# Optimization experiments

Hardware: AMD Instinct MI355X
Metric: run time of the kernel (lower is better)

Reference implementation:

```python
import jax, jax.numpy as jnp
import numpy as np

MARGIN = 1.0
EPS = 1e-8


def setup_inputs() -> dict:
    key = jax.random.key(0)
    k1, k2 = jax.random.split(key)
    B, D, NUM_CLASSES = 8192, 512, 100
    features = jax.random.normal(k1, (B, D), dtype=jnp.float32)
    labels = jax.random.randint(k2, (B,), 0, NUM_CLASSES, dtype=jnp.int64)
    return {"features": features, "labels": labels}


def _metric_tensor(features):
    # G = I + feature covariance (curvature-aware metric on the feature manifold)
    B, D = features.shape
    centered = features - jnp.mean(features, axis=0, keepdims=True)
    cov = jnp.einsum('bi,bj->ij', centered, centered) / jnp.float32(B)
    return jnp.eye(D, dtype=features.dtype) + cov


def _masked_random_idx(mask, key):
    # gumbel-max trick: uniform random index among True entries of each row of mask [B,B]
    g = -jnp.log(-jnp.log(jax.random.uniform(key, mask.shape, dtype=jnp.float32) + EPS) + EPS)
    scores = jnp.where(mask, g, -jnp.inf)
    return jnp.argmax(scores, axis=1)


def reference(features, labels):
    B = features.shape[0]
    G = _metric_tensor(features)

    same = labels[:, None] == labels[None, :]              # [B,B]
    not_self = ~jnp.eye(B, dtype=bool)
    pos_mask = same & not_self
    neg_mask = ~same

    kp, kn = jax.random.split(jax.random.key(42))
    pos_idx = _masked_random_idx(pos_mask, kp)             # [B]
    neg_idx = _masked_random_idx(neg_mask, kn)             # [B]
    valid = jnp.any(pos_mask, axis=1) & jnp.any(neg_mask, axis=1)

    diff_p = features - features[pos_idx]                  # [B,D]
    diff_n = features - features[neg_idx]                  # [B,D]
    # Riemannian distance: sqrt((x-y)^T G (x-y))
    d_pos = jnp.sqrt(jnp.einsum('bi,ij,bj->b', diff_p, G, diff_p) + EPS)
    d_neg = jnp.sqrt(jnp.einsum('bi,ij,bj->b', diff_n, G, diff_n) + EPS)

    per_sample = jnp.maximum(d_pos - d_neg + MARGIN, 0.0)
    per_sample = jnp.where(valid, per_sample, 0.0)
    n_valid = jnp.maximum(jnp.sum(valid.astype(jnp.float32)), 1.0)
    return jnp.sum(per_sample) / n_valid
```

## Files before the change

### kernel.cpp

```cpp
#include <hip/hip_runtime.h>
#include <stdint.h>

#define BSZ   8192
#define DIM   512

typedef __attribute__((ext_vector_type(8))) short short8;
typedef __attribute__((ext_vector_type(4))) float f32x4;
typedef __attribute__((ext_vector_type(8))) uint16_t u16x8;

__host__ __device__ inline uint16_t f2bf(float x) {
  uint32_t u = __float_as_uint(x);
  return (uint16_t)((u + 0x7FFFu + ((u >> 16) & 1u)) >> 16);
}
__host__ __device__ inline float bf2f(uint16_t h) {
  return __uint_as_float(((uint32_t)h) << 16);
}

__host__ __device__ inline uint32_t rotl32(uint32_t v, int s) {
#if defined(__HIP_DEVICE_COMPILE__) && __has_builtin(__builtin_amdgcn_alignbit)
  return __builtin_amdgcn_alignbit(v, v, 32 - s);
#else
  return (v << s) | (v >> (32 - s));
#endif
}

__host__ __device__ inline void threefry2x32(uint32_t k0, uint32_t k1,
                                             uint32_t x0, uint32_t x1,
                                             uint32_t& o0, uint32_t& o1) {
  uint32_t ks2 = k0 ^ k1 ^ 0x1BD11BDAu;
  x0 += k0; x1 += k1;
  x0 += x1; x1 = rotl32(x1, 13); x1 ^= x0;
  x0 += x1; x1 = rotl32(x1, 15); x1 ^= x0;
  x0 += x1; x1 = rotl32(x1, 26); x1 ^= x0;
  x0 += x1; x1 = rotl32(x1,  6); x1 ^= x0;
  x0 += k1; x1 += ks2 + 1u;
  x0 += x1; x1 = rotl32(x1, 17); x1 ^= x0;
  x0 += x1; x1 = rotl32(x1, 29); x1 ^= x0;
  x0 += x1; x1 = rotl32(x1, 16); x1 ^= x0;
  x0 += x1; x1 = rotl32(x1, 24); x1 ^= x0;
  x0 += ks2; x1 += k0 + 2u;
  x0 += x1; x1 = rotl32(x1, 13); x1 ^= x0;
  x0 += x1; x1 = rotl32(x1, 15); x1 ^= x0;
  x0 += x1; x1 = rotl32(x1, 26); x1 ^= x0;
  x0 += x1; x1 = rotl32(x1,  6); x1 ^= x0;
  x0 += k0; x1 += k1 + 3u;
  x0 += x1; x1 = rotl32(x1, 17); x1 ^= x0;
  x0 += x1; x1 = rotl32(x1, 29); x1 ^= x0;
  x0 += x1; x1 = rotl32(x1, 16); x1 ^= x0;
  x0 += x1; x1 = rotl32(x1, 24); x1 ^= x0;
  x0 += k1; x1 += ks2 + 4u;
  x0 += x1; x1 = rotl32(x1, 13); x1 ^= x0;
  x0 += x1; x1 = rotl32(x1, 15); x1 ^= x0;
  x0 += x1; x1 = rotl32(x1, 26); x1 ^= x0;
  x0 += x1; x1 = rotl32(x1,  6); x1 ^= x0;
  x0 += ks2; x1 += k0 + 5u;
  o0 = x0; o1 = x1;
}

constexpr size_t OFF_ACC    = 0;
constexpr size_t OFF_S      = 1024;
constexpr size_t OFF_BSTART = 3072;
constexpr size_t OFF_BIDX   = 4096;
constexpr size_t OFF_PIDX   = 36864;
constexpr size_t OFF_NIDX   = 69632;
constexpr size_t OFF_LPART  = 102400;
constexpr size_t OFF_GB     = 131072;
constexpr size_t OFF_FB     = 2097152;
constexpr size_t OFF_HB     = 10485760;
constexpr size_t ZERO_BYTES = 3072;

__global__ __launch_bounds__(256) void convert_kernel(const float* __restrict__ F,
                                                      uint16_t* __restrict__ Fb) {
  int i = (blockIdx.x * 256 + threadIdx.x) * 8;
  float4 a = *(const float4*)&F[i];
  float4 b = *(const float4*)&F[i + 4];
  u16x8 o;
  o[0] = f2bf(a.x); o[1] = f2bf(a.y); o[2] = f2bf(a.z); o[3] = f2bf(a.w);
  o[4] = f2bf(b.x); o[5] = f2bf(b.y); o[6] = f2bf(b.z); o[7] = f2bf(b.w);
  *(u16x8*)&Fb[i] = o;
}

__global__ __launch_bounds__(256) void colsum_kernel(const float* __restrict__ F,
                                                     float* __restrict__ S) {
  int b0 = blockIdx.x * 32;
  int t = threadIdx.x;
  float s0 = 0.f, s1 = 0.f;
  for (int r = 0; r < 32; ++r) {
    const float* row = F + (size_t)(b0 + r) * DIM;
    s0 += row[t];
    s1 += row[t + 256];
  }
  atomicAdd(&S[t], s0);
  atomicAdd(&S[t + 256], s1);
}

__global__ __launch_bounds__(256) void covmat_mfma_kernel(const uint16_t* __restrict__ Fb,
                                                          float* __restrict__ Mpart) {
  __shared__ uint16_t sA[64][40];
  __shared__ uint16_t sB[64][40];
  int i0 = blockIdx.x * 64;
  int j0 = blockIdx.y * 64;
  int kc0 = blockIdx.z * 2048;
  int tid = threadIdx.x;
  int lane = tid & 63, wid = tid >> 6, quad = lane >> 4, l16 = lane & 15;
  int wm = (wid >> 1) * 32;
  int wn = (wid & 1) * 32;
  int sk = tid & 31;
  int sm = (tid >> 5) * 8;
  f32x4 acc[2][2] = {};
  for (int kk = 0; kk < 2048; kk += 32) {
    int krow = kc0 + kk + sk;
    u16x8 va = *(const u16x8*)&Fb[(size_t)krow * DIM + i0 + sm];
    u16x8 vb = *(const u16x8*)&Fb[(size_t)krow * DIM + j0 + sm];
    __syncthreads();
#pragma unroll
    for (int jj = 0; jj < 8; ++jj) { sA[sm + jj][sk] = va[jj]; sB[sm + jj][sk] = vb[jj]; }
    __syncthreads();
#pragma unroll
    for (int r = 0; r < 2; ++r) {
      short8 af = *(short8*)&sA[wm + r * 16 + l16][quad * 8];
#pragma unroll
      for (int c = 0; c < 2; ++c) {
        short8 bf = *(short8*)&sB[wn + c * 16 + l16][quad * 8];
        acc[r][c] = __builtin_amdgcn_mfma_f32_16x16x32_bf16(af, bf, acc[r][c], 0, 0, 0);
      }
    }
  }
  float* out = Mpart + (size_t)blockIdx.z * DIM * DIM;
#pragma unroll
  for (int r = 0; r < 2; ++r)
#pragma unroll
    for (int c = 0; c < 2; ++c)
#pragma unroll
      for (int g = 0; g < 4; ++g)
        out[(size_t)(i0 + wm + r * 16 + quad * 4 + g) * DIM + j0 + wn + c * 16 + l16] = acc[r][c][g];
}

__global__ __launch_bounds__(256) void buildG_kernel(const float* __restrict__ Mpart,
                                                     const float* __restrict__ S,
                                                     uint16_t* __restrict__ Gb) {
  int idx = blockIdx.x * 256 + threadIdx.x;
  int i = idx >> 9, j = idx & 511;
  float m = Mpart[idx] + Mpart[(size_t)DIM * DIM + idx] +
            Mpart[2 * (size_t)DIM * DIM + idx] + Mpart[3 * (size_t)DIM * DIM + idx];
  const float invB = 1.0f / (float)BSZ;
  float mi = S[i] * invB, mj = S[j] * invB;
  float g = m * invB - mi * mj + (i == j ? 1.0f : 0.0f);
  Gb[idx] = f2bf(g);
}

__global__ __launch_bounds__(256) void matmulH_mfma_kernel(const uint16_t* __restrict__ Fb,
                                                           const uint16_t* __restrict__ Gb,
                                                           uint16_t* __restrict__ Hb) {
  __shared__ uint16_t sA[128][72];
  __shared__ uint16_t sB[64][72];
  int n0 = blockIdx.x * 64;
  int m0 = blockIdx.y * 128;
  int tid = threadIdx.x;
  int lane = tid & 63, wid = tid >> 6, quad = lane >> 4, l16 = lane & 15;
  int am = tid & 127, ah = (tid >> 7) * 32;
  int bk = tid >> 2, bn = (tid & 3) * 16;
  f32x4 acc[2][4] = {};
  for (int k0 = 0; k0 < DIM; k0 += 64) {
    __syncthreads();
    {
      const uint16_t* src = &Fb[(size_t)(m0 + am) * DIM + k0 + ah];
#pragma unroll
      for (int v = 0; v < 4; ++v)
        *(u16x8*)&sA[am][ah + v * 8] = *(const u16x8*)&src[v * 8];
    }
    {
      u16x8 g0 = *(const u16x8*)&Gb[(size_t)(k0 + bk) * DIM + n0 + bn];
      u16x8 g1 = *(const u16x8*)&Gb[(size_t)(k0 + bk) * DIM + n0 + bn + 8];
#pragma unroll
      for (int jj = 0; jj < 8; ++jj) { sB[bn + jj][bk] = g0[jj]; sB[bn + 8 + jj][bk] = g1[jj]; }
    }
    __syncthreads();
#pragma unroll
    for (int k32 = 0; k32 < 64; k32 += 32) {
      short8 af[2];
#pragma unroll
      for (int r = 0; r < 2; ++r)
        af[r] = *(short8*)&sA[wid * 32 + r * 16 + l16][k32 + quad * 8];
#pragma unroll
      for (int c = 0; c < 4; ++c) {
        short8 bf = *(short8*)&sB[c * 16 + l16][k32 + quad * 8];
#pragma unroll
        for (int r = 0; r < 2; ++r)
          acc[r][c] = __builtin_amdgcn_mfma_f32_16x16x32_bf16(af[r], bf, acc[r][c], 0, 0, 0);
      }
    }
  }
#pragma unroll
  for (int r = 0; r < 2; ++r)
#pragma unroll
    for (int c = 0; c < 4; ++c)
#pragma unroll
      for (int g = 0; g < 4; ++g) {
        int row = m0 + wid * 32 + r * 16 + quad * 4 + g;
        int col = n0 + c * 16 + l16;
        Hb[(size_t)row * DIM + col] = f2bf(acc[r][c][g]);
      }
}

__global__ __launch_bounds__(256) void bucket_kernel(const int* __restrict__ labels,
                                                     int* __restrict__ bucketStart,
                                                     int* __restrict__ bucketIdx) {
  __shared__ int cnt[128];
  __shared__ int base[128];
  int tid = threadIdx.x;
  if (tid < 128) cnt[tid] = 0;
  __syncthreads();
  for (int b = tid; b < BSZ; b += 256) atomicAdd(&cnt[labels[b]], 1);
  __syncthreads();
  if (tid == 0) {
    int run = 0;
    for (int c = 0; c < 100; ++c) { base[c] = run; bucketStart[c] = run; run += cnt[c]; }
    bucketStart[100] = run;
  }
  __syncthreads();
  for (int b = tid; b < BSZ; b += 256) {
    int p = atomicAdd(&base[labels[b]], 1);
    bucketIdx[p] = b;
  }
}

__global__ __launch_bounds__(256) void negmax_kernel(const int* __restrict__ labels,
                                                     uint32_t kn0, uint32_t kn1,
                                                     int* __restrict__ negIdx) {
  __shared__ __align__(16) uint8_t slab[BSZ];
  __shared__ unsigned long long wmax[4];
  int tid = threadIdx.x;
  {
    uint32_t* s32 = (uint32_t*)slab;
#pragma unroll
    for (int pass = 0; pass < 8; ++pass) {
      int idx = pass * 1024 + tid * 4;
      int4 l4 = *(const int4*)&labels[idx];
      uint32_t packed = (uint32_t)(l4.x & 0xFF) | ((uint32_t)(l4.y & 0xFF) << 8) |
                        ((uint32_t)(l4.z & 0xFF) << 16) | ((uint32_t)(l4.w & 0xFF) << 24);
      s32[pass * 256 + tid] = packed;
    }
  }
  __syncthreads();
  int i = blockIdx.x;
  uint32_t li = slab[i];
  uint32_t base = (uint32_t)(i << 13);
  unsigned long long bA = 0, bB = 0, bC = 0, bD = 0;
#pragma unroll 2
  for (int it = 0; it < 8; ++it) {
    int c0 = tid + (it << 10);
    int c1 = c0 + 256;
    int c2 = c0 + 512;
    int c3 = c0 + 768;
    uint32_t l0 = slab[c0], l1 = slab[c1], l2 = slab[c2], l3 = slab[c3];
    uint32_t a0, a1, e0, e1, f0, f1, g0, g1;
    threefry2x32(kn0, kn1, 0u, base + (uint32_t)c0, a0, a1);
    threefry2x32(kn0, kn1, 0u, base + (uint32_t)c1, e0, e1);
    threefry2x32(kn0, kn1, 0u, base + (uint32_t)c2, f0, f1);
    threefry2x32(kn0, kn1, 0u, base + (uint32_t)c3, g0, g1);
    unsigned long long compA = ((unsigned long long)((a0 ^ a1) >> 9) << 32) | (uint32_t)(~c0);
    unsigned long long compB = ((unsigned long long)((e0 ^ e1) >> 9) << 32) | (uint32_t)(~c1);
    unsigned long long compC = ((unsigned long long)((f0 ^ f1) >> 9) << 32) | (uint32_t)(~c2);
    unsigned long long compD = ((unsigned long long)((g0 ^ g1) >> 9) << 32) | (uint32_t)(~c3);
    if (l0 == li) compA = 0;
    if (l1 == li) compB = 0;
    if (l2 == li) compC = 0;
    if (l3 == li) compD = 0;
    if (compA > bA) bA = compA;
    if (compB > bB) bB = compB;
    if (compC > bC) bC = compC;
    if (compD > bD) bD = compD;
  }
  if (bB > bA) bA = bB;
  if (bC > bA) bA = bC;
  if (bD > bA) bA = bD;
  unsigned long long best = bA;
#pragma unroll
  for (int off = 32; off; off >>= 1) {
    unsigned long long o = __shfl_down(best, off);
    if (o > best) best = o;
  }
  int wid = tid >> 6;
  if ((tid & 63) == 0) wmax[wid] = best;
  __syncthreads();
  if (tid == 0) {
    best = wmax[0];
    for (int w = 1; w < 4; ++w) if (wmax[w] > best) best = wmax[w];
    negIdx[i] = best ? (int)(~(uint32_t)best) : -1;
  }
}

__global__ __launch_bounds__(256) void posmax_kernel(const int* __restrict__ labels,
                                                     const int* __restrict__ bucketStart,
                                                     const int* __restrict__ bucketIdx,
                                                     uint32_t kp0, uint32_t kp1,
                                                     int* __restrict__ posIdx) {
  int row = blockIdx.x * 4 + (threadIdx.x >> 6);
  int lane = threadIdx.x & 63;
  int cls = labels[row];
  int s = bucketStart[cls], e = bucketStart[cls + 1];
  uint32_t base = (uint32_t)(row << 13);
  unsigned long long best = 0;
  for (int t = s + lane; t < e; t += 64) {
    int cc = bucketIdx[t];
    uint32_t a0, a1;
    threefry2x32(kp0, kp1, 0u, base + (uint32_t)cc, a0, a1);
    uint32_t bits = (a0 ^ a1) >> 9;
    unsigned long long comp = ((unsigned long long)bits << 32) | (uint32_t)(~cc);
    if (cc == row) comp = 0;
    if (comp > best) best = comp;
  }
#pragma unroll
  for (int off = 32; off; off >>= 1) {
    unsigned long long o = __shfl_down(best, off);
    if (o > best) best = o;
  }
  if (lane == 0) posIdx[row] = best ? (int)(~(uint32_t)best) : -1;
}

__global__ __launch_bounds__(256) void loss_kernel(const float* __restrict__ F,
                                                   const uint16_t* __restrict__ Hb,
                                                   const int* __restrict__ posIdx,
                                                   const int* __restrict__ negIdx,
                                                   float2* __restrict__ lossPart) {
  __shared__ float2 part[4];
  int row = blockIdx.x * 4 + (threadIdx.x >> 6);
  int lane = threadIdx.x & 63;
  int p = posIdx[row], n = negIdx[row];
  bool valid = (p >= 0) && (n >= 0);
  int ps = valid ? p : row;
  int ns = valid ? n : row;
  int k = lane * 8;
  const float* Fi = F + (size_t)row * DIM + k;
  const float* Fp = F + (size_t)ps * DIM + k;
  const float* Fn = F + (size_t)ns * DIM + k;
  const uint16_t* Hi = Hb + (size_t)row * DIM + k;
  const uint16_t* Hp = Hb + (size_t)ps * DIM + k;
  const uint16_t* Hn = Hb + (size_t)ns * DIM + k;
  float4 fi0 = *(const float4*)&Fi[0], fi1 = *(const float4*)&Fi[4];
  float4 fp0 = *(const float4*)&Fp[0], fp1 = *(const float4*)&Fp[4];
  float4 fn0 = *(const float4*)&Fn[0], fn1 = *(const float4*)&Fn[4];
  u16x8 h_i = *(const u16x8*)Hi;
  u16x8 h_p = *(const u16x8*)Hp;
  u16x8 h_n = *(const u16x8*)Hn;
  float fi[8] = {fi0.x, fi0.y, fi0.z, fi0.w, fi1.x, fi1.y, fi1.z, fi1.w};
  float fp[8] = {fp0.x, fp0.y, fp0.z, fp0.w, fp1.x, fp1.y, fp1.z, fp1.w};
  float fn[8] = {fn0.x, fn0.y, fn0.z, fn0.w, fn1.x, fn1.y, fn1.z, fn1.w};
  float qii = 0.f, qpp = 0.f, qip = 0.f, qnn = 0.f, qin = 0.f;
#pragma unroll
  for (int jj = 0; jj < 8; ++jj) {
    float hi = bf2f(h_i[jj]), hp = bf2f(h_p[jj]), hn = bf2f(h_n[jj]);
    qii += fi[jj] * hi;
    qpp += fp[jj] * hp;
    qip += fi[jj] * hp;
    qnn += fn[jj] * hn;
    qin += fi[jj] * hn;
  }
#pragma unroll
  for (int off = 32; off > 0; off >>= 1) {
    qii += __shfl_down(qii, off);
    qpp += __shfl_down(qpp, off);
    qip += __shfl_down(qip, off);
    qnn += __shfl_down(qnn, off);
    qin += __shfl_down(qin, off);
  }
  if (lane == 0) {
    float d2p = fmaxf(qii + qpp - 2.f * qip, 0.f);
    float d2n = fmaxf(qii + qnn - 2.f * qin, 0.f);
    float dpos = sqrtf(d2p + 1e-8f);
    float dneg = sqrtf(d2n + 1e-8f);
    float v = fmaxf(dpos - dneg + 1.0f, 0.0f);
    if (!valid) v = 0.f;
    part[threadIdx.x >> 6] = make_float2(v, valid ? 1.f : 0.f);
  }
  __syncthreads();
  if (threadIdx.x == 0) {
    float s = 0.f, c = 0.f;
#pragma unroll
    for (int w = 0; w < 4; ++w) { s += part[w].x; c += part[w].y; }
    lossPart[blockIdx.x] = make_float2(s, c);
  }
}

__global__ __launch_bounds__(256) void finalize_kernel(const float2* __restrict__ lossPart,
                                                       float* __restrict__ out) {
  __shared__ float2 wsum[4];
  int tid = threadIdx.x;
  float s = 0.f, c = 0.f;
  for (int z = tid; z < 2048; z += 256) {
    float2 v = lossPart[z];
    s += v.x; c += v.y;
  }
#pragma unroll
  for (int off = 32; off > 0; off >>= 1) {
    s += __shfl_down(s, off);
    c += __shfl_down(c, off);
  }
  if ((tid & 63) == 0) wsum[tid >> 6] = make_float2(s, c);
  __syncthreads();
  if (tid == 0) {
    s = 0.f; c = 0.f;
#pragma unroll
    for (int w = 0; w < 4; ++w) { s += wsum[w].x; c += wsum[w].y; }
    out[0] = s / fmaxf(c, 1.0f);
  }
}

extern "C" void kernel_launch(void* const* d_in, const int* in_sizes, int n_in,
                              void* d_out, int out_size, void* d_ws, size_t ws_size,
                              hipStream_t stream) {
  const float* F = (const float*)d_in[0];
  const int* labels = (const int*)d_in[1];
  float* out = (float*)d_out;
  char* ws = (char*)d_ws;

  float* S       = (float*)(ws + OFF_S);
  int* bStart    = (int*)(ws + OFF_BSTART);
  int* bIdx      = (int*)(ws + OFF_BIDX);
  int* posIdx    = (int*)(ws + OFF_PIDX);
  int* negIdx    = (int*)(ws + OFF_NIDX);
  float2* lPart  = (float2*)(ws + OFF_LPART);
  uint16_t* Gb   = (uint16_t*)(ws + OFF_GB);
  uint16_t* Fb   = (uint16_t*)(ws + OFF_FB);
  uint16_t* Hb   = (uint16_t*)(ws + OFF_HB);
  float* Mpart   = (float*)(ws + OFF_HB);

  uint32_t kp0, kp1, kn0, kn1;
  threefry2x32(0u, 42u, 0u, 0u, kp0, kp1);
  threefry2x32(0u, 42u, 0u, 1u, kn0, kn1);

  hipMemsetAsync(ws, 0, ZERO_BYTES, stream);

  convert_kernel<<<2048, 256, 0, stream>>>(F, Fb);

  colsum_kernel<<<256, 256, 0, stream>>>(F, S);

  dim3 covGrid(8, 8, 4);
  covmat_mfma_kernel<<<covGrid, 256, 0, stream>>>(Fb, Mpart);

  buildG_kernel<<<(DIM * DIM) / 256, 256, 0, stream>>>(Mpart, S, Gb);

  bucket_kernel<<<1, 256, 0, stream>>>(labels, bStart, bIdx);

  negmax_kernel<<<BSZ, 256, 0, stream>>>(labels, kn0, kn1, negIdx);

  posmax_kernel<<<BSZ / 4, 256, 0, stream>>>(labels, bStart, bIdx, kp0, kp1, posIdx);

  dim3 hGrid(8, 64);
  matmulH_mfma_kernel<<<hGrid, 256, 0, stream>>>(Fb, Gb, Hb);

  loss_kernel<<<BSZ / 4, 256, 0, stream>>>(F, Hb, posIdx, negIdx, lPart);

  finalize_kernel<<<1, 256, 0, stream>>>(lPart, out);
}
```

Baseline: 347.1 us.

## Merge matmul, positive and negative sampling into one persistent overlap kernel

Three kernels become one launch of 1024 blocks. The first 224 blocks compute the H = F·G tiles with a grid-stride loop, the next 32 handle positive sampling, and every block then takes negative-sampling rows from an atomic work counter. Separately, the column-sum kernel is folded into the bf16 convert kernel. The aim is to run the MFMA matmul alongside the threefry-heavy negative sampling and to cut launch gaps. The cost is a persistent-style schedule that depends on the zeroed counter, a shared-memory union, and an extra barrier per row.

Result: faster. 332.1 us (-4.3%).

```diff
diff --git a/kernel.cpp b/kernel.cpp
--- a/kernel.cpp
+++ b/kernel.cpp
@@ -57,7 +57,7 @@
   o0 = x0; o1 = x1;
 }
 
-constexpr size_t OFF_ACC    = 0;
+constexpr size_t OFF_CTR    = 0;
 constexpr size_t OFF_S      = 1024;
 constexpr size_t OFF_BSTART = 3072;
 constexpr size_t OFF_BIDX   = 4096;
@@ -69,8 +69,9 @@
 constexpr size_t OFF_HB     = 10485760;
 constexpr size_t ZERO_BYTES = 3072;
 
-__global__ __launch_bounds__(256) void convert_kernel(const float* __restrict__ F,
-                                                      uint16_t* __restrict__ Fb) {
+__global__ __launch_bounds__(256) void prep_kernel(const float* __restrict__ F,
+                                                   uint16_t* __restrict__ Fb,
+                                                   float* __restrict__ S) {
   int i = (blockIdx.x * 256 + threadIdx.x) * 8;
   float4 a = *(const float4*)&F[i];
   float4 b = *(const float4*)&F[i + 4];
@@ -78,20 +79,18 @@
   o[0] = f2bf(a.x); o[1] = f2bf(a.y); o[2] = f2bf(a.z); o[3] = f2bf(a.w);
   o[4] = f2bf(b.x); o[5] = f2bf(b.y); o[6] = f2bf(b.z); o[7] = f2bf(b.w);
   *(u16x8*)&Fb[i] = o;
-}
-
-__global__ __launch_bounds__(256) void colsum_kernel(const float* __restrict__ F,
-                                                     float* __restrict__ S) {
-  int b0 = blockIdx.x * 32;
-  int t = threadIdx.x;
-  float s0 = 0.f, s1 = 0.f;
-  for (int r = 0; r < 32; ++r) {
-    const float* row = F + (size_t)(b0 + r) * DIM;
-    s0 += row[t];
-    s1 += row[t + 256];
-  }
-  atomicAdd(&S[t], s0);
-  atomicAdd(&S[t + 256], s1);
+  if (blockIdx.x < 256) {
+    int b0 = blockIdx.x * 32;
+    int t = threadIdx.x;
+    float s0 = 0.f, s1 = 0.f;
+    for (int r = 0; r < 32; ++r) {
+      const float* row = F + (size_t)(b0 + r) * DIM;
+      s0 += row[t];
+      s1 += row[t + 256];
+    }
+    atomicAdd(&S[t], s0);
+    atomicAdd(&S[t + 256], s1);
+  }
 }
 
 __global__ __launch_bounds__(256) void covmat_mfma_kernel(const uint16_t* __restrict__ Fb,
@@ -145,62 +144,7 @@
             Mpart[2 * (size_t)DIM * DIM + idx] + Mpart[3 * (size_t)DIM * DIM + idx];
   const float invB = 1.0f / (float)BSZ;
   float mi = S[i] * invB, mj = S[j] * invB;
-  float g = m * invB - mi * mj + (i == j ? 1.0f : 0.0f);
-  Gb[idx] = f2bf(g);
-}
-
-__global__ __launch_bounds__(256) void matmulH_mfma_kernel(const uint16_t* __restrict__ Fb,
-                                                           const uint16_t* __restrict__ Gb,
-                                                           uint16_t* __restrict__ Hb) {
-  __shared__ uint16_t sA[128][72];
-  __shared__ uint16_t sB[64][72];
-  int n0 = blockIdx.x * 64;
-  int m0 = blockIdx.y * 128;
-  int tid = threadIdx.x;
-  int lane = tid & 63, wid = tid >> 6, quad = lane >> 4, l16 = lane & 15;
-  int am = tid & 127, ah = (tid >> 7) * 32;
-  int bk = tid >> 2, bn = (tid & 3) * 16;
-  f32x4 acc[2][4] = {};
-  for (int k0 = 0; k0 < DIM; k0 += 64) {
-    __syncthreads();
-    {
-      const uint16_t* src = &Fb[(size_t)(m0 + am) * DIM + k0 + ah];
-#pragma unroll
-      for (int v = 0; v < 4; ++v)
-        *(u16x8*)&sA[am][ah + v * 8] = *(const u16x8*)&src[v * 8];
-    }
-    {
-      u16x8 g0 = *(const u16x8*)&Gb[(size_t)(k0 + bk) * DIM + n0 + bn];
-      u16x8 g1 = *(const u16x8*)&Gb[(size_t)(k0 + bk) * DIM + n0 + bn + 8];
-#pragma unroll
-      for (int jj = 0; jj < 8; ++jj) { sB[bn + jj][bk] = g0[jj]; sB[bn + 8 + jj][bk] = g1[jj]; }
-    }
-    __syncthreads();
-#pragma unroll
-    for (int k32 = 0; k32 < 64; k32 += 32) {
-      short8 af[2];
-#pragma unroll
-      for (int r = 0; r < 2; ++r)
-        af[r] = *(short8*)&sA[wid * 32 + r * 16 + l16][k32 + quad * 8];
-#pragma unroll
-      for (int c = 0; c < 4; ++c) {
-        short8 bf = *(short8*)&sB[c * 16 + l16][k32 + quad * 8];
-#pragma unroll
-        for (int r = 0; r < 2; ++r)
-          acc[r][c] = __builtin_amdgcn_mfma_f32_16x16x32_bf16(af[r], bf, acc[r][c], 0, 0, 0);
-      }
-    }
-  }
-#pragma unroll
-  for (int r = 0; r < 2; ++r)
-#pragma unroll
-    for (int c = 0; c < 4; ++c)
-#pragma unroll
-      for (int g = 0; g < 4; ++g) {
-        int row = m0 + wid * 32 + r * 16 + quad * 4 + g;
-        int col = n0 + c * 16 + l16;
-        Hb[(size_t)row * DIM + col] = f2bf(acc[r][c][g]);
-      }
+  Gb[idx] = f2bf(m * invB - mi * mj + (i == j ? 1.0f : 0.0f));
 }
 
 __global__ __launch_bounds__(256) void bucket_kernel(const int* __restrict__ labels,
@@ -225,14 +169,94 @@
   }
 }
 
-__global__ __launch_bounds__(256) void negmax_kernel(const int* __restrict__ labels,
-                                                     uint32_t kn0, uint32_t kn1,
-                                                     int* __restrict__ negIdx) {
-  __shared__ __align__(16) uint8_t slab[BSZ];
-  __shared__ unsigned long long wmax[4];
-  int tid = threadIdx.x;
+struct SharedMM  { uint16_t sA[128][72]; uint16_t sB[64][72]; };
+struct SharedNeg { uint8_t slab[BSZ]; unsigned long long wmax[4]; int curRow; };
+union __align__(16) SharedU { SharedMM mm; SharedNeg neg; };
+
+__global__ __launch_bounds__(256) void overlap_kernel(
+    const uint16_t* __restrict__ Fb, const uint16_t* __restrict__ Gb,
+    uint16_t* __restrict__ Hb, const int* __restrict__ labels,
+    const int* __restrict__ bStart, const int* __restrict__ bIdx,
+    int* __restrict__ posIdx, int* __restrict__ negIdx,
+    int* __restrict__ rowCtr,
+    uint32_t kp0, uint32_t kp1, uint32_t kn0, uint32_t kn1) {
+  __shared__ SharedU sh;
+  int bid = blockIdx.x, tid = threadIdx.x;
+  int lane = tid & 63, wid = tid >> 6, quad = lane >> 4, l16 = lane & 15;
+
+  if (bid < 224) {
+    int am = tid & 127, ah = (tid >> 7) * 32;
+    int bk = tid >> 2, bn = (tid & 3) * 16;
+    int tm = wid * 32;
+    for (int t = bid; t < 512; t += 224) {
+      int n0 = (t & 7) * 64;
+      int m0 = (t >> 3) * 128;
+      f32x4 acc[2][4] = {};
+      for (int k0 = 0; k0 < DIM; k0 += 64) {
+        {
+          const uint16_t* src = &Fb[(size_t)(m0 + am) * DIM + k0 + ah];
+#pragma unroll
+          for (int v = 0; v < 4; ++v)
+            *(u16x8*)&sh.mm.sA[am][ah + v * 8] = *(const u16x8*)&src[v * 8];
+        }
+        {
+          u16x8 g0 = *(const u16x8*)&Gb[(size_t)(k0 + bk) * DIM + n0 + bn];
+          u16x8 g1 = *(const u16x8*)&Gb[(size_t)(k0 + bk) * DIM + n0 + bn + 8];
+#pragma unroll
+          for (int jj = 0; jj < 8; ++jj) { sh.mm.sB[bn + jj][bk] = g0[jj]; sh.mm.sB[bn + 8 + jj][bk] = g1[jj]; }
+        }
+        __syncthreads();
+#pragma unroll
+        for (int k32 = 0; k32 < 64; k32 += 32) {
+          short8 af[2];
+#pragma unroll
+          for (int r = 0; r < 2; ++r)
+            af[r] = *(short8*)&sh.mm.sA[tm + r * 16 + l16][k32 + quad * 8];
+#pragma unroll
+          for (int c = 0; c < 4; ++c) {
+            short8 bf = *(short8*)&sh.mm.sB[c * 16 + l16][k32 + quad * 8];
+#pragma unroll
+            for (int r = 0; r < 2; ++r)
+              acc[r][c] = __builtin_amdgcn_mfma_f32_16x16x32_bf16(af[r], bf, acc[r][c], 0, 0, 0);
+          }
+        }
+        __syncthreads();
+      }
+#pragma unroll
+      for (int r = 0; r < 2; ++r)
+#pragma unroll
+        for (int c = 0; c < 4; ++c)
+#pragma unroll
+          for (int g = 0; g < 4; ++g)
+            Hb[(size_t)(m0 + tm + r * 16 + quad * 4 + g) * DIM + n0 + c * 16 + l16] = f2bf(acc[r][c][g]);
+    }
+    __syncthreads();
+  } else if (bid < 256) {
+    for (int row = (bid - 224) * 4 + wid; row < BSZ; row += 128) {
+      int cls = labels[row];
+      int s = bStart[cls], e = bStart[cls + 1];
+      uint32_t base = (uint32_t)(row << 13);
+      unsigned long long best = 0;
+      for (int t2 = s + lane; t2 < e; t2 += 64) {
+        int cc = bIdx[t2];
+        uint32_t a0, a1;
+        threefry2x32(kp0, kp1, 0u, base + (uint32_t)cc, a0, a1);
+        unsigned long long comp = ((unsigned long long)((a0 ^ a1) >> 9) << 32) | (uint32_t)(~cc);
+        if (cc == row) comp = 0;
+        if (comp > best) best = comp;
+      }
+#pragma unroll
+      for (int off = 32; off; off >>= 1) {
+        unsigned long long o = __shfl_down(best, off);
+        if (o > best) best = o;
+      }
+      if (lane == 0) posIdx[row] = best ? (int)(~(uint32_t)best) : -1;
+    }
+    __syncthreads();
+  }
+
   {
-    uint32_t* s32 = (uint32_t*)slab;
+    uint32_t* s32 = (uint32_t*)sh.neg.slab;
 #pragma unroll
     for (int pass = 0; pass < 8; ++pass) {
       int idx = pass * 1024 + tid * 4;
@@ -243,80 +267,55 @@
     }
   }
   __syncthreads();
-  int i = blockIdx.x;
-  uint32_t li = slab[i];
-  uint32_t base = (uint32_t)(i << 13);
-  unsigned long long bA = 0, bB = 0, bC = 0, bD = 0;
+  while (true) {
+    if (tid == 0) sh.neg.curRow = atomicAdd(rowCtr, 1);
+    __syncthreads();
+    int row = sh.neg.curRow;
+    if (row >= BSZ) break;
+    uint32_t li = sh.neg.slab[row];
+    uint32_t base = (uint32_t)(row << 13);
+    unsigned long long bA = 0, bB = 0, bC = 0, bD = 0;
 #pragma unroll 2
-  for (int it = 0; it < 8; ++it) {
-    int c0 = tid + (it << 10);
-    int c1 = c0 + 256;
-    int c2 = c0 + 512;
-    int c3 = c0 + 768;
-    uint32_t l0 = slab[c0], l1 = slab[c1], l2 = slab[c2], l3 = slab[c3];
-    uint32_t a0, a1, e0, e1, f0, f1, g0, g1;
-    threefry2x32(kn0, kn1, 0u, base + (uint32_t)c0, a0, a1);
-    threefry2x32(kn0, kn1, 0u, base + (uint32_t)c1, e0, e1);
-    threefry2x32(kn0, kn1, 0u, base + (uint32_t)c2, f0, f1);
-    threefry2x32(kn0, kn1, 0u, base + (uint32_t)c3, g0, g1);
-    unsigned long long compA = ((unsigned long long)((a0 ^ a1) >> 9) << 32) | (uint32_t)(~c0);
-    unsigned long long compB = ((unsigned long long)((e0 ^ e1) >> 9) << 32) | (uint32_t)(~c1);
-    unsigned long long compC = ((unsigned long long)((f0 ^ f1) >> 9) << 32) | (uint32_t)(~c2);
-    unsigned long long compD = ((unsigned long long)((g0 ^ g1) >> 9) << 32) | (uint32_t)(~c3);
-    if (l0 == li) compA = 0;
-    if (l1 == li) compB = 0;
-    if (l2 == li) compC = 0;
-    if (l3 == li) compD = 0;
-    if (compA > bA) bA = compA;
-    if (compB > bB) bB = compB;
-    if (compC > bC) bC = compC;
-    if (compD > bD) bD = compD;
-  }
-  if (bB > bA) bA = bB;
-  if (bC > bA) bA = bC;
-  if (bD > bA) bA = bD;
-  unsigned long long best = bA;
-#pragma unroll
-  for (int off = 32; off; off >>= 1) {
-    unsigned long long o = __shfl_down(best, off);
-    if (o > best) best = o;
-  }
-  int wid = tid >> 6;
-  if ((tid & 63) == 0) wmax[wid] = best;
-  __syncthreads();
-  if (tid == 0) {
-    best = wmax[0];
-    for (int w = 1; w < 4; ++w) if (wmax[w] > best) best = wmax[w];
-    negIdx[i] = best ? (int)(~(uint32_t)best) : -1;
-  }
-}
-
-__global__ __launch_bounds__(256) void posmax_kernel(const int* __restrict__ labels,
-                                                     const int* __restrict__ bucketStart,
-                                                     const int* __restrict__ bucketIdx,
-                                                     uint32_t kp0, uint32_t kp1,
-                                                     int* __restrict__ posIdx) {
-  int row = blockIdx.x * 4 + (threadIdx.x >> 6);
-  int lane = threadIdx.x & 63;
-  int cls = labels[row];
-  int s = bucketStart[cls], e = bucketStart[cls + 1];
-  uint32_t base = (uint32_t)(row << 13);
-  unsigned long long best = 0;
-  for (int t = s + lane; t < e; t += 64) {
-    int cc = bucketIdx[t];
-    uint32_t a0, a1;
-    threefry2x32(kp0, kp1, 0u, base + (uint32_t)cc, a0, a1);
-    uint32_t bits = (a0 ^ a1) >> 9;
-    unsigned long long comp = ((unsigned long long)bits << 32) | (uint32_t)(~cc);
-    if (cc == row) comp = 0;
-    if (comp > best) best = comp;
-  }
-#pragma unroll
-  for (int off = 32; off; off >>= 1) {
-    unsigned long long o = __shfl_down(best, off);
-    if (o > best) best = o;
-  }
-  if (lane == 0) posIdx[row] = best ? (int)(~(uint32_t)best) : -1;
+    for (int it = 0; it < 8; ++it) {
+      int c0 = tid + (it << 10);
+      int c1 = c0 + 256, c2 = c0 + 512, c3 = c0 + 768;
+      uint32_t l0 = sh.neg.slab[c0], l1 = sh.neg.slab[c1], l2 = sh.neg.slab[c2], l3 = sh.neg.slab[c3];
+      uint32_t a0, a1, e0, e1, f0, f1, g0, g1;
+      threefry2x32(kn0, kn1, 0u, base + (uint32_t)c0, a0, a1);
+      threefry2x32(kn0, kn1, 0u, base + (uint32_t)c1, e0, e1);
+      threefry2x32(kn0, kn1, 0u, base + (uint32_t)c2, f0, f1);
+      threefry2x32(kn0, kn1, 0u, base + (uint32_t)c3, g0, g1);
+      unsigned long long compA = ((unsigned long long)((a0 ^ a1) >> 9) << 32) | (uint32_t)(~c0);
+      unsigned long long compB = ((unsigned long long)((e0 ^ e1) >> 9) << 32) | (uint32_t)(~c1);
+      unsigned long long compC = ((unsigned long long)((f0 ^ f1) >> 9) << 32) | (uint32_t)(~c2);
+      unsigned long long compD = ((unsigned long long)((g0 ^ g1) >> 9) << 32) | (uint32_t)(~c3);
+      if (l0 == li) compA = 0;
+      if (l1 == li) compB = 0;
+      if (l2 == li) compC = 0;
+      if (l3 == li) compD = 0;
+      if (compA > bA) bA = compA;
+      if (compB > bB) bB = compB;
+      if (compC > bC) bC = compC;
+      if (compD > bD) bD = compD;
+    }
+    if (bB > bA) bA = bB;
+    if (bC > bA) bA = bC;
+    if (bD > bA) bA = bD;
+    unsigned long long best = bA;
+#pragma unroll
+    for (int off = 32; off; off >>= 1) {
+      unsigned long long o = __shfl_down(best, off);
+      if (o > best) best = o;
+    }
+    if (lane == 0) sh.neg.wmax[wid] = best;
+    __syncthreads();
+    if (tid == 0) {
+      best = sh.neg.wmax[0];
+      for (int w = 1; w < 4; ++w) if (sh.neg.wmax[w] > best) best = sh.neg.wmax[w];
+      negIdx[row] = best ? (int)(~(uint32_t)best) : -1;
+    }
+    __syncthreads();
+  }
 }
 
 __global__ __launch_bounds__(256) void loss_kernel(const float* __restrict__ F,
@@ -335,15 +334,12 @@
   const float* Fi = F + (size_t)row * DIM + k;
   const float* Fp = F + (size_t)ps * DIM + k;
   const float* Fn = F + (size_t)ns * DIM + k;
-  const uint16_t* Hi = Hb + (size_t)row * DIM + k;
-  const uint16_t* Hp = Hb + (size_t)ps * DIM + k;
-  const uint16_t* Hn = Hb + (size_t)ns * DIM + k;
+  u16x8 h_i = *(const u16x8*)(Hb + (size_t)row * DIM + k);
+  u16x8 h_p = *(const u16x8*)(Hb + (size_t)ps * DIM + k);
+  u16x8 h_n = *(const u16x8*)(Hb + (size_t)ns * DIM + k);
   float4 fi0 = *(const float4*)&Fi[0], fi1 = *(const float4*)&Fi[4];
   float4 fp0 = *(const float4*)&Fp[0], fp1 = *(const float4*)&Fp[4];
   float4 fn0 = *(const float4*)&Fn[0], fn1 = *(const float4*)&Fn[4];
-  u16x8 h_i = *(const u16x8*)Hi;
-  u16x8 h_p = *(const u16x8*)Hp;
-  u16x8 h_n = *(const u16x8*)Hn;
   float fi[8] = {fi0.x, fi0.y, fi0.z, fi0.w, fi1.x, fi1.y, fi1.z, fi1.w};
   float fp[8] = {fp0.x, fp0.y, fp0.z, fp0.w, fp1.x, fp1.y, fp1.z, fp1.w};
   float fn[8] = {fn0.x, fn0.y, fn0.z, fn0.w, fn1.x, fn1.y, fn1.z, fn1.w};
@@ -368,9 +364,7 @@
   if (lane == 0) {
     float d2p = fmaxf(qii + qpp - 2.f * qip, 0.f);
     float d2n = fmaxf(qii + qnn - 2.f * qin, 0.f);
-    float dpos = sqrtf(d2p + 1e-8f);
-    float dneg = sqrtf(d2n + 1e-8f);
-    float v = fmaxf(dpos - dneg + 1.0f, 0.0f);
+    float v = fmaxf(sqrtf(d2p + 1e-8f) - sqrtf(d2n + 1e-8f) + 1.0f, 0.0f);
     if (!valid) v = 0.f;
     part[threadIdx.x >> 6] = make_float2(v, valid ? 1.f : 0.f);
   }
@@ -415,6 +409,7 @@
   float* out = (float*)d_out;
   char* ws = (char*)d_ws;
 
+  int* rowCtr    = (int*)(ws + OFF_CTR);
   float* S       = (float*)(ws + OFF_S);
   int* bStart    = (int*)(ws + OFF_BSTART);
   int* bIdx      = (int*)(ws + OFF_BIDX);
@@ -432,9 +427,7 @@
 
   hipMemsetAsync(ws, 0, ZERO_BYTES, stream);
 
-  convert_kernel<<<2048, 256, 0, stream>>>(F, Fb);
-
-  colsum_kernel<<<256, 256, 0, stream>>>(F, S);
+  prep_kernel<<<2048, 256, 0, stream>>>(F, Fb, S);
 
   dim3 covGrid(8, 8, 4);
   covmat_mfma_kernel<<<covGrid, 256, 0, stream>>>(Fb, Mpart);
@@ -443,12 +436,9 @@
 
   bucket_kernel<<<1, 256, 0, stream>>>(labels, bStart, bIdx);
 
-  negmax_kernel<<<BSZ, 256, 0, stream>>>(labels, kn0, kn1, negIdx);
-
-  posmax_kernel<<<BSZ / 4, 256, 0, stream>>>(labels, bStart, bIdx, kp0, kp1, posIdx);
-
-  dim3 hGrid(8, 64);
-  matmulH_mfma_kernel<<<hGrid, 256, 0, stream>>>(Fb, Gb, Hb);
+  overlap_kernel<<<1024, 256, 0, stream>>>(Fb, Gb, Hb, labels, bStart, bIdx,
+                                           posIdx, negIdx, rowCtr,
+                                           kp0, kp1, kn0, kn1);
 
   loss_kernel<<<BSZ / 4, 256, 0, stream>>>(F, Hb, posIdx, negIdx, lPart);
 
```
